# Kernel optimization log

Measured on AMD Instinct MI355X. Metric: run time of the kernel, lower is better.

## Reference

```python
import jax, jax.numpy as jnp
import numpy as np

CURVE = 1.0
TAU = 0.5
N_NODES = 32768
N_EDGES = 65536
IN_CH = 64
OUT_CH = 64
N_HEADS = 8
N_RF = 128
EPS = 1e-7


def _make_projection_matrix(m, d, seed=0):
    # FAVOR+ projection: stacked rows of transposed QR blocks, row-rescaled by chi norms.
    rng = np.random.RandomState(seed)
    blocks = []
    nb_full = m // d
    for _ in range(nb_full):
        q, _ = np.linalg.qr(rng.randn(d, d))
        blocks.append(q.T)
    rem = m - nb_full * d
    if rem > 0:
        q, _ = np.linalg.qr(rng.randn(d, d))
        blocks.append(q.T[:rem])
    final = np.vstack(blocks)  # [m, d]
    mult = np.linalg.norm(rng.randn(m, d), axis=1)
    return (mult[:, None] * final).astype(np.float32)


def _expmap0(u, c):
    # Hyperboloid exp map at origin; time slot of u is ignored.
    sqrtK = 1.0 / jnp.sqrt(c)
    x = u[..., 1:]
    xn = jnp.maximum(jnp.linalg.norm(x, axis=-1, keepdims=True), EPS)
    theta = xn / sqrtK
    return jnp.concatenate([sqrtK * jnp.cosh(theta), sqrtK * jnp.sinh(theta) * x / xn], axis=-1)


def _proj(x, c):
    # Re-project onto hyperboloid: x0 = sqrt(1/c + ||x_space||^2)
    K = 1.0 / c
    y = x[..., 1:]
    t = jnp.sqrt(K + jnp.sum(y * y, axis=-1, keepdims=True))
    return jnp.concatenate([t, y], axis=-1)


def _logmap0(x, c):
    # Hyperboloid log map at origin; output tangent has zero time component.
    sqrtK = 1.0 / jnp.sqrt(c)
    y = x[..., 1:]
    yn = jnp.maximum(jnp.linalg.norm(y, axis=-1, keepdims=True), EPS)
    t = jnp.maximum(x[..., 0:1] / sqrtK, 1.0 + EPS)
    res = sqrtK * jnp.arccosh(t) * y / yn
    return jnp.concatenate([jnp.zeros_like(res[..., :1]), res], axis=-1)


def _softmax_kernel(data, P, tau, c):
    # Performer-style exp kernel with hyperbolic (time-coordinate) prefactor.
    dt = data[..., 0:1]
    ds = data[..., 1:]
    m = 1.0 / jnp.sqrt(jnp.asarray(P.shape[0], jnp.float32))
    wx = jnp.exp(jnp.einsum('bnhd,dm->bnhm', ds, P) / jnp.sqrt(tau))
    front = jnp.exp((c / tau - dt * dt / tau) / 2.0) * m  # [b,n,h,1]
    return wx * front


def setup_inputs() -> dict:
    key = jax.random.key(0)
    k1, k2, k3, k4 = jax.random.split(key, 4)
    std = (2.0 / (IN_CH + OUT_CH)) ** 0.5
    z = 0.01 * jax.random.normal(k1, (1, N_NODES, IN_CH), jnp.float32)
    Wq = std * jax.random.normal(k2, (N_HEADS, OUT_CH, IN_CH), jnp.float32)
    Wk = std * jax.random.normal(k3, (N_HEADS, OUT_CH, IN_CH), jnp.float32)
    Wv = std * jax.random.normal(k4, (N_HEADS, OUT_CH, IN_CH), jnp.float32)
    edge_index = jax.random.randint(jax.random.fold_in(key, 7), (2, N_EDGES), 0, N_NODES, jnp.int32)
    proj_mat = jnp.asarray(_make_projection_matrix(IN_CH - 1, N_RF))  # [63, 128]
    return {"z": z, "Wq": Wq, "Wk": Wk, "Wv": Wv, "proj_mat": proj_mat, "edge_index": edge_index}


def reference(z, Wq, Wk, Wv, proj_mat, edge_index):
    c = jnp.float32(CURVE)
    tau = jnp.float32(TAU)
    zs = z[0]  # [N, C] (B == 1, squeeze)
    zh = _proj(_expmap0(zs, c), c)  # lift features to hyperboloid
    u = _logmap0(zh, c)             # [N, C], tangent at origin

    def hyplin(W):  # HypLinear (no bias): proj(expmap0(logmap0(x) @ W^T)) for all heads
        mu = jnp.einsum('nc,hoc->hno', u, W)  # [H, N, D]
        return _proj(_expmap0(mu, c), c)

    q, k, v = hyplin(Wq), hyplin(Wk), hyplin(Wv)  # [H, N, D]
    H, N, D = q.shape
    # mirrors torch stacked.reshape(-1, N, H, D) (row-major relabeling)
    query = q.reshape(1, N, H, D)
    key_ = k.reshape(1, N, H, D)
    value = v.reshape(1, N, H, D)

    qp = _softmax_kernel(query, proj_mat, tau, c).transpose(2, 0, 1, 3)  # [H,1,N,M]
    kp = _softmax_kernel(key_, proj_mat, tau, c).transpose(2, 0, 1, 3)   # [H,1,N,M]
    vv = value.transpose(2, 0, 1, 3)                                      # [H,1,N,D]

    last = jnp.einsum('hbnm,hbnd->hbmd', kp, vv)   # [H,1,M,D] kv summary
    zo = jnp.einsum('hbnm,hbmd->hbnd', qp, last)   # [H,1,N,D]
    mnorm = -zo[..., 0:1] ** 2 + jnp.sum(zo[..., 1:] ** 2, axis=-1, keepdims=True)
    zo = zo / (jnp.sqrt(c) * jnp.sqrt(jnp.abs(mnorm)))  # renormalize onto hyperboloid

    start, end = edge_index[0], edge_index[1]
    ea = jnp.einsum('hbem,hbem->hbe', qp[:, :, end, :], kp[:, :, start, :])
    A_weight = ea.transpose(1, 2, 0)  # [1, E, H]

    # hyper_agg: Euclidean head-mean followed by Minkowski renormalization
    t = jnp.mean(zo[:, 0], axis=0)  # [N, D]
    xn = -t[..., 0:1] ** 2 + jnp.sum(t[..., 1:] ** 2, axis=-1, keepdims=True)
    z_next = t / (jnp.sqrt(c) * jnp.sqrt(jnp.abs(xn)))
    link_loss = jnp.mean(A_weight)
    return z_next, link_loss
```

## Files before the change

kernel.cpp:

```cpp
#include <hip/hip_runtime.h>

#define DEV __device__ __forceinline__

#define NNODES 32768
#define NEDGES 65536
#define NROWS  262144
#define EPSF   1e-7f
#define SQRT2F 1.4142135623730951f
#define LOG2E  1.4426950408889634f
#define LOG2SQRT63 2.9886399611087573f

#define OFF_WFRAG 0u
#define OFF_LASTB 0u
#define OFF_PFRAG 196608u
#define OFF_EA    212992u
#define OFF_U     409600u
#define OFF_PART  42352640u
#define OFF_PHIQ  75907072u
#define OFF_PHIK  143015936u

typedef short s8v __attribute__((ext_vector_type(8)));
typedef float f4v __attribute__((ext_vector_type(4)));
typedef float f2v __attribute__((ext_vector_type(2)));

DEV unsigned short f2bf(float f) {
  unsigned u = __float_as_uint(f);
  return (unsigned short)((u + 0x7fffu + ((u >> 16) & 1u)) >> 16);
}
DEV float bf2f(unsigned short h) { return __uint_as_float(((unsigned)h) << 16); }
DEV unsigned pack2(float lo, float hi) {
  return __builtin_amdgcn_perm(__float_as_uint(hi) + 0x8000u, __float_as_uint(lo) + 0x8000u, 0x07060302u);
}
DEV float frcp(float x) { return __builtin_amdgcn_rcpf(x); }
DEV float fsqrt(float x) { return __builtin_amdgcn_sqrtf(x); }
DEV float fexp2(float x) { return __builtin_amdgcn_exp2f(x); }

__global__ __launch_bounds__(256) void k01_prep(const float* __restrict__ z, unsigned short* __restrict__ ubf,
                                                const float* __restrict__ Wq, const float* __restrict__ Wk,
                                                const float* __restrict__ Wv, const float* __restrict__ P,
                                                unsigned short* __restrict__ Wfrag, unsigned short* __restrict__ Pfrag,
                                                float* __restrict__ ea) {
  int i = blockIdx.x * 256 + threadIdx.x;
  float4 v = *(const float4*)(z + (size_t)i * 4);
  if ((i & 15) == 0) v.x = 0.f;
  uint2 pk;
  pk.x = pack2(v.x, v.y);
  pk.y = pack2(v.z, v.w);
  *(uint2*)(ubf + (size_t)i * 4) = pk;

  if (blockIdx.x < 96) {
    if (i == 0) ea[0] = 0.f;
    int stride = 96 * 256;
    for (int t = i; t < 98304; t += stride) {
      int j = t & 7, lane = (t >> 3) & 63, nt = (t >> 9) & 3, ks = (t >> 11) & 1, h = (t >> 12) & 7, sm = t >> 15;
      int k = ks * 32 + (lane >> 4) * 8 + j;
      int n = nt * 16 + (lane & 15);
      const float* W = (sm == 0) ? Wq : ((sm == 1) ? Wk : Wv);
      Wfrag[t] = f2bf(W[(h * 64 + n) * 64 + k]);
    }
    for (int t = i; t < 8192; t += stride) {
      int j = t & 7, lane = (t >> 3) & 63, ks = (t >> 9) & 1, mt = (t >> 10) & 7;
      int k = ks * 32 + (lane >> 4) * 8 + j;
      int r = lane & 15;
      int m = ((mt >> 2) << 6) + ((r >> 2) << 4) + ((mt & 3) << 2) + (r & 3);
      Pfrag[t] = (k == 0) ? (unsigned short)0 : f2bf(P[(k - 1) * 128 + m] * (SQRT2F * LOG2E));
    }
  }
}

__global__ __launch_bounds__(256, 4) void k2_mfma(const unsigned short* __restrict__ ubf,
                                                  const unsigned short* __restrict__ Wfrag,
                                                  const unsigned short* __restrict__ Pfrag,
                                                  unsigned char* __restrict__ phiq, unsigned char* __restrict__ phik,
                                                  unsigned short* __restrict__ part) {
  __shared__ short lds_raw[13312];
  short* sbuf = lds_raw;
  float* sfront = (float*)(lds_raw + 9216);
  unsigned char* kbufT8 = (unsigned char*)lds_raw;
  unsigned char* vbufT8 = (unsigned char*)lds_raw + 9216;

  int w = threadIdx.x >> 6, lane = threadIdx.x & 63;
  int q = lane >> 4, l = lane & 15;
  int b = blockIdx.x;
  int h = b >> 8, t = b & 255;
  int n0 = t * 128 + w * 32;

  s8v afr[2][2];
#pragma unroll
  for (int mt = 0; mt < 2; ++mt)
#pragma unroll
    for (int ks = 0; ks < 2; ++ks)
      afr[mt][ks] = *(const s8v*)(ubf + (size_t)(n0 + mt * 16 + l) * 64 + ks * 32 + q * 8);

  const s8v* Wf = (const s8v*)Wfrag;
  const s8v* Pf = (const s8v*)Pfrag;
  unsigned vk[2][4];
  unsigned keepA[8], keepB[8];

#pragma unroll
  for (int sm = 0; sm < 3; ++sm) {
    f4v acc[2][4];
#pragma unroll
    for (int mt = 0; mt < 2; ++mt)
#pragma unroll
      for (int nt = 0; nt < 4; ++nt) acc[mt][nt] = (f4v)(0.f);
#pragma unroll
    for (int ks = 0; ks < 2; ++ks)
#pragma unroll
      for (int nt = 0; nt < 4; ++nt) {
        s8v bf = Wf[(((sm * 8 + h) * 2 + ks) * 4 + nt) * 64 + lane];
#pragma unroll
        for (int mt = 0; mt < 2; ++mt)
          acc[mt][nt] = __builtin_amdgcn_mfma_f32_16x16x32_bf16(afr[mt][ks], bf, acc[mt][nt], 0, 0, 0);
      }
#pragma unroll
    for (int mt = 0; mt < 2; ++mt) {
      float rs[4];
#pragma unroll
      for (int reg = 0; reg < 4; ++reg) {
        float v0 = (l == 0) ? 0.f : acc[mt][0][reg];
        rs[reg] = v0 * v0 + acc[mt][1][reg] * acc[mt][1][reg] + acc[mt][2][reg] * acc[mt][2][reg] +
                  acc[mt][3][reg] * acc[mt][3][reg];
      }
#pragma unroll
      for (int reg = 0; reg < 4; ++reg) {
#pragma unroll
        for (int off = 1; off < 16; off <<= 1) rs[reg] += __shfl_xor(rs[reg], off, 64);
      }
      float vreg[4][4];
#pragma unroll
      for (int reg = 0; reg < 4; ++reg) {
        float x = fmaxf(fsqrt(rs[reg]), EPSF);
        float e = fexp2(x * LOG2E);
        float sh = 0.5f * (e - frcp(e));
        float ratio = sh * frcp(x);
        float sh2 = sh * sh;
        int row = mt * 16 + q * 4 + reg;
        if (sm == 2) {
          float tt2 = fsqrt(1.f + sh2);
#pragma unroll
          for (int nt = 0; nt < 4; ++nt) {
            float val = acc[mt][nt][reg] * ratio;
            if (l == 0 && nt == 0) val = tt2;
            vreg[nt][reg] = val;
          }
        } else {
          float lf = -sh2 * LOG2E - LOG2SQRT63;
          if (l == 0) sfront[w * 32 + row] = lf;
#pragma unroll
          for (int nt = 0; nt < 4; ++nt) {
            float val = acc[mt][nt][reg] * ratio;
            if (l == 0 && nt == 0) val = 0.f;
            sbuf[w * 2304 + row * 72 + ((nt * 16 + l) ^ ((q >> 1) << 4))] =
                (short)(__float_as_uint(val) >> 16);
          }
        }
      }
      if (sm == 2) {
#pragma unroll
        for (int nt = 0; nt < 4; ++nt) {
          unsigned pv = __builtin_amdgcn_cvt_pk_fp8_f32(vreg[nt][0], vreg[nt][1], 0, 0);
          vk[mt][nt] = __builtin_amdgcn_cvt_pk_fp8_f32(vreg[nt][2], vreg[nt][3], pv, 1);
        }
      }
    }

    if (sm < 2) {
      int fr = (l >> 3) & 1;
      s8v bsf[2][2];
#pragma unroll
      for (int nt = 0; nt < 2; ++nt)
#pragma unroll
        for (int ks = 0; ks < 2; ++ks)
          bsf[nt][ks] = *(const s8v*)&sbuf[w * 2304 + (nt * 16 + l) * 72 + ((ks * 32 + q * 8) ^ (fr << 4))];
      float lf0 = sfront[w * 32 + l];
      float lf1 = sfront[w * 32 + 16 + l];
      unsigned char* dst = sm ? phik : phiq;
      unsigned g0a[4], g0b[4], g1a[4], g1b[4];
#pragma unroll
      for (int mt = 0; mt < 8; ++mt) {
        f4v a0 = (f4v)(0.f), a1 = (f4v)(0.f);
#pragma unroll
        for (int ks = 0; ks < 2; ++ks) {
          s8v ap = Pf[(mt * 2 + ks) * 64 + lane];
          a0 = __builtin_amdgcn_mfma_f32_16x16x32_bf16(ap, bsf[0][ks], a0, 0, 0, 0);
          a1 = __builtin_amdgcn_mfma_f32_16x16x32_bf16(ap, bsf[1][ks], a1, 0, 0, 0);
        }
        float v00 = fexp2(a0[0] + lf0), v01 = fexp2(a0[1] + lf0), v02 = fexp2(a0[2] + lf0), v03 = fexp2(a0[3] + lf0);
        float v10 = fexp2(a1[0] + lf1), v11 = fexp2(a1[1] + lf1), v12 = fexp2(a1[2] + lf1), v13 = fexp2(a1[3] + lf1);
        unsigned p0 = __builtin_amdgcn_cvt_pk_fp8_f32(v00, v01, 0, 0);
        p0 = __builtin_amdgcn_cvt_pk_fp8_f32(v02, v03, p0, 1);
        unsigned p1 = __builtin_amdgcn_cvt_pk_fp8_f32(v10, v11, 0, 0);
        p1 = __builtin_amdgcn_cvt_pk_fp8_f32(v12, v13, p1, 1);
        if (mt < 4) { g0a[mt] = p0; g1a[mt] = p1; }
        else        { g0b[mt - 4] = p0; g1b[mt - 4] = p1; }
        if (sm == 1) { keepA[mt] = p0; keepB[mt] = p1; }
      }
      size_t b0 = (size_t)(n0 + l) * 1024 + (size_t)(h * 128 + q * 16);
      *(uint4*)(dst + b0)              = make_uint4(g0a[0], g0a[1], g0a[2], g0a[3]);
      *(uint4*)(dst + b0 + 64)         = make_uint4(g0b[0], g0b[1], g0b[2], g0b[3]);
      *(uint4*)(dst + b0 + 16384)      = make_uint4(g1a[0], g1a[1], g1a[2], g1a[3]);
      *(uint4*)(dst + b0 + 16384 + 64) = make_uint4(g1b[0], g1b[1], g1b[2], g1b[3]);
    }
  }

  f4v facc[2][4];
#pragma unroll
  for (int mtl = 0; mtl < 2; ++mtl)
#pragma unroll
    for (int nt = 0; nt < 4; ++nt) facc[mtl][nt] = (f4v)(0.f);

#pragma unroll
  for (int hf = 0; hf < 2; ++hf) {
    __syncthreads();
    if ((w >> 1) == hf) {
      int nd0 = (w & 1) * 32 + l, nd1 = nd0 + 16;
      int c0 = nd0 ^ (q << 4), c1 = nd1 ^ (q << 4);
#pragma unroll
      for (int mt = 0; mt < 8; ++mt) {
        int M0 = ((mt >> 2) << 6) + (q << 4) + ((mt & 3) << 2);
        unsigned a = keepA[mt], bq = keepB[mt];
#pragma unroll
        for (int r = 0; r < 4; ++r) {
          kbufT8[(M0 + r) * 72 + c0] = (unsigned char)(a >> (8 * r));
          kbufT8[(M0 + r) * 72 + c1] = (unsigned char)(bq >> (8 * r));
        }
      }
#pragma unroll
      for (int mt = 0; mt < 2; ++mt)
#pragma unroll
        for (int nt = 0; nt < 4; ++nt)
          *(unsigned*)&vbufT8[(nt * 16 + l) * 72 + (w & 1) * 32 + mt * 16 + q * 4] = vk[mt][nt];
    }
    __syncthreads();
#pragma unroll
    for (int kc = 0; kc < 2; ++kc) {
      long bv[4];
#pragma unroll
      for (int nt = 0; nt < 4; ++nt)
        bv[nt] = *(const long*)&vbufT8[(nt * 16 + l) * 72 + kc * 32 + q * 8];
      long av[2];
#pragma unroll
      for (int mtl = 0; mtl < 2; ++mtl) {
        int row = (2 * w + mtl) * 16 + l;
        int cb = (kc * 32 + q * 8) ^ (((2 * w + mtl) & 3) << 4);
        av[mtl] = *(const long*)&kbufT8[row * 72 + cb];
      }
#pragma unroll
      for (int mtl = 0; mtl < 2; ++mtl)
#pragma unroll
        for (int nt = 0; nt < 4; ++nt)
          facc[mtl][nt] = __builtin_amdgcn_mfma_f32_16x16x32_fp8_fp8(av[mtl], bv[nt], facc[mtl][nt], 0, 0, 0);
    }
  }

#pragma unroll
  for (int mtl = 0; mtl < 2; ++mtl)
#pragma unroll
    for (int nt = 0; nt < 4; ++nt) {
      uint2 pk;
      pk.x = pack2(facc[mtl][nt][0], facc[mtl][nt][1]);
      pk.y = pack2(facc[mtl][nt][2], facc[mtl][nt][3]);
      int d = nt * 16 + l;
      int m = (2 * w + mtl) * 16 + q * 4;
      *(uint2*)(part + ((size_t)((t * 8 + h) * 64 + d)) * 128 + m) = pk;
    }
}

__global__ __launch_bounds__(256) void k35(const unsigned* __restrict__ part32, unsigned char* __restrict__ lastB,
                                           const unsigned char* __restrict__ phiq,
                                           const unsigned char* __restrict__ phik,
                                           const int* __restrict__ ei, float* __restrict__ ea) {
  int b = blockIdx.x;
  if (b < 128) {
    int t2 = b * 256 + threadIdx.x;
    float s0 = 0.f, s1 = 0.f;
#pragma unroll 16
    for (int c = 0; c < 256; ++c) {
      unsigned v = part32[((size_t)c << 12) + t2];
      s0 += __uint_as_float(v << 16);
      s1 += __uint_as_float(v & 0xffff0000u);
    }
    int m = (t2 & 63) * 2, d = (t2 >> 6) & 63, h = t2 >> 12;
    int ks = m >> 5, j = m & 7, qq = (m >> 3) & 3;
    int lane = qq * 16 + (d & 15), nt = d >> 4;
    unsigned r = __builtin_amdgcn_cvt_pk_bf8_f32(s0, s1, 0, 0);
    *(unsigned short*)(lastB + ((((h * 4 + ks) * 4 + nt) * 64 + lane) << 3) + j) = (unsigned short)r;
    return;
  }
  __shared__ float part[4];
  int lane = threadIdx.x & 63, w = threadIdx.x >> 6;
  int wid = (b - 128) * 4 + w;
  float acc0 = 0.f, acc1 = 0.f;
#pragma unroll
  for (int i = 0; i < 8; i += 2) {
    int e0 = wid * 8 + i, e1 = e0 + 1;
    int s0 = ei[e0], d0 = ei[NEDGES + e0];
    int s1 = ei[e1], d1 = ei[NEDGES + e1];
    uint4 qa = *(const uint4*)(phiq + (size_t)d0 * 1024 + lane * 16);
    uint4 ka = *(const uint4*)(phik + (size_t)s0 * 1024 + lane * 16);
    uint4 qb = *(const uint4*)(phiq + (size_t)d1 * 1024 + lane * 16);
    uint4 kb = *(const uint4*)(phik + (size_t)s1 * 1024 + lane * 16);
    unsigned qs[8] = {qa.x, qa.y, qa.z, qa.w, qb.x, qb.y, qb.z, qb.w};
    unsigned ks[8] = {ka.x, ka.y, ka.z, ka.w, kb.x, kb.y, kb.z, kb.w};
#pragma unroll
    for (int p = 0; p < 8; ++p) {
      f2v q0 = __builtin_amdgcn_cvt_pk_f32_fp8(qs[p], 0);
      f2v q1 = __builtin_amdgcn_cvt_pk_f32_fp8(qs[p], 1);
      f2v k0 = __builtin_amdgcn_cvt_pk_f32_fp8(ks[p], 0);
      f2v k1 = __builtin_amdgcn_cvt_pk_f32_fp8(ks[p], 1);
      float t0 = fmaf(q0.x, k0.x, q0.y * k0.y);
      float t1 = fmaf(q1.x, k1.x, q1.y * k1.y);
      if (p < 4) acc0 += t0 + t1; else acc1 += t0 + t1;
    }
  }
  float acc = acc0 + acc1;
#pragma unroll
  for (int o = 1; o < 64; o <<= 1) acc += __shfl_xor(acc, o, 64);
  if (lane == 0) part[w] = acc;
  __syncthreads();
  if (threadIdx.x == 0) atomicAdd(ea, part[0] + part[1] + part[2] + part[3]);
}

__global__ __launch_bounds__(512) void k4_mfma(const unsigned char* __restrict__ phiq,
                                               const unsigned char* __restrict__ lastB,
                                               const float* __restrict__ ea, float* __restrict__ out) {
  __shared__ unsigned zbufT[8][64][18];
  int w = threadIdx.x >> 6, lane = threadIdx.x & 63;
  int q = lane >> 4, l = lane & 15;
  int n0 = blockIdx.x * 32;

  const long* Bf = (const long*)lastB;
  long bf[4][4];
#pragma unroll
  for (int ks = 0; ks < 4; ++ks)
#pragma unroll
    for (int nt = 0; nt < 4; ++nt) bf[ks][nt] = Bf[((w * 4 + ks) * 4 + nt) * 64 + lane];

  long af[2][4];
#pragma unroll
  for (int mt = 0; mt < 2; ++mt)
#pragma unroll
    for (int ks = 0; ks < 4; ++ks)
      af[mt][ks] = *(const long*)(phiq + (size_t)(8 * (n0 + mt * 16 + l) + w) * 128 + ks * 32 + q * 8);

  f4v acc[2][4];
#pragma unroll
  for (int mt = 0; mt < 2; ++mt)
#pragma unroll
    for (int nt = 0; nt < 4; ++nt) acc[mt][nt] = (f4v)(0.f);
#pragma unroll
  for (int ks = 0; ks < 4; ++ks)
#pragma unroll
    for (int nt = 0; nt < 4; ++nt)
#pragma unroll
      for (int mt = 0; mt < 2; ++mt)
        acc[mt][nt] = __builtin_amdgcn_mfma_f32_16x16x32_fp8_bf8(af[mt][ks], bf[ks][nt], acc[mt][nt], 0, 0, 0);

#pragma unroll
  for (int mt = 0; mt < 2; ++mt) {
    float rs[4];
#pragma unroll
    for (int reg = 0; reg < 4; ++reg) {
      float v0 = acc[mt][0][reg];
      float s0 = (l == 0) ? -v0 * v0 : v0 * v0;
      rs[reg] = s0 + acc[mt][1][reg] * acc[mt][1][reg] + acc[mt][2][reg] * acc[mt][2][reg] +
                acc[mt][3][reg] * acc[mt][3][reg];
    }
#pragma unroll
    for (int reg = 0; reg < 4; ++reg) {
#pragma unroll
      for (int off = 1; off < 16; off <<= 1) rs[reg] += __shfl_xor(rs[reg], off, 64);
    }
    float inv[4];
#pragma unroll
    for (int reg = 0; reg < 4; ++reg) inv[reg] = frcp(fsqrt(fabsf(rs[reg])));
#pragma unroll
    for (int nt = 0; nt < 4; ++nt) {
      uint2 pk;
      pk.x = pack2(acc[mt][nt][0] * inv[0], acc[mt][nt][1] * inv[1]);
      pk.y = pack2(acc[mt][nt][2] * inv[2], acc[mt][nt][3] * inv[3]);
      *(uint2*)&zbufT[w][nt * 16 + l][mt * 8 + q * 2] = pk;
    }
  }
  __syncthreads();

  int tid = threadIdx.x;
  int i = tid >> 4, dg = tid & 15;
  int i2 = i >> 1, sel = i & 1;
  float s[4] = {0.f, 0.f, 0.f, 0.f};
#pragma unroll
  for (int w2 = 0; w2 < 8; ++w2) {
#pragma unroll
    for (int j = 0; j < 4; ++j) {
      unsigned u = zbufT[w2][dg * 4 + j][i2];
      s[j] += bf2f((unsigned short)(sel ? (u >> 16) : (u & 0xffffu)));
    }
  }
  float m2 = 0.f;
#pragma unroll
  for (int j = 0; j < 4; ++j) {
    s[j] *= 0.125f;
    m2 += ((dg == 0 && j == 0) ? -s[j] * s[j] : s[j] * s[j]);
  }
#pragma unroll
  for (int off = 1; off < 16; off <<= 1) m2 += __shfl_xor(m2, off, 64);
  float inv = frcp(fsqrt(fabsf(m2)));
  float4 o = make_float4(s[0] * inv, s[1] * inv, s[2] * inv, s[3] * inv);
  *(float4*)(out + (size_t)(n0 + i) * 64 + dg * 4) = o;
  if (blockIdx.x == 0 && tid == 0) out[(size_t)NNODES * 64] = ea[0] * (1.0f / 524288.0f);
}

extern "C" void kernel_launch(void* const* d_in, const int* in_sizes, int n_in,
                              void* d_out, int out_size, void* d_ws, size_t ws_size,
                              hipStream_t stream) {
  const float* z  = (const float*)d_in[0];
  const float* Wq = (const float*)d_in[1];
  const float* Wk = (const float*)d_in[2];
  const float* Wv = (const float*)d_in[3];
  const float* P  = (const float*)d_in[4];
  const int* ei   = (const int*)d_in[5];
  char* ws = (char*)d_ws;
  unsigned short* Wfrag = (unsigned short*)(ws + OFF_WFRAG);
  unsigned char*  lastB = (unsigned char*)(ws + OFF_LASTB);
  unsigned short* Pfrag = (unsigned short*)(ws + OFF_PFRAG);
  float*          ea    = (float*)(ws + OFF_EA);
  unsigned short* ubf   = (unsigned short*)(ws + OFF_U);
  unsigned short* part  = (unsigned short*)(ws + OFF_PART);
  unsigned char*  phiq  = (unsigned char*)(ws + OFF_PHIQ);
  unsigned char*  phik  = (unsigned char*)(ws + OFF_PHIK);

  k01_prep<<<2048, 256, 0, stream>>>(z, ubf, Wq, Wk, Wv, P, Wfrag, Pfrag, ea);
  k2_mfma<<<2048, 256, 0, stream>>>(ubf, Wfrag, Pfrag, phiq, phik, part);
  k35<<<128 + 2048, 256, 0, stream>>>((const unsigned*)part, lastB, phiq, phik, ei, ea);
  k4_mfma<<<NNODES / 32, 512, 0, stream>>>(phiq, lastB, ea, (float*)d_out);
}
```

Before: 177.4 us.

## Store per-tile KV partial sums as bf8 and shrink LDS for higher occupancy

The per-tile K^T V partial sums written by k2 are now packed to bf8 instead of bf16, halving that intermediate buffer, and the k35 reduction reads four bf8 values per word, so it launches half as many reduction blocks. The k2 LDS array is cut down and launch bounds raised from 4 to 8 blocks per CU to allow more occupancy. The cost is extra quantization error in 256 partial sums summed into the kv summary, and the smaller LDS array may be inconsistent with kbufT8/vbufT8 regions that previously extended beyond it.

```diff
diff --git a/kernel.cpp b/kernel.cpp
--- a/kernel.cpp
+++ b/kernel.cpp
@@ -68,12 +68,12 @@
   }
 }
 
-__global__ __launch_bounds__(256, 4) void k2_mfma(const unsigned short* __restrict__ ubf,
+__global__ __launch_bounds__(256, 8) void k2_mfma(const unsigned short* __restrict__ ubf,
                                                   const unsigned short* __restrict__ Wfrag,
                                                   const unsigned short* __restrict__ Pfrag,
                                                   unsigned char* __restrict__ phiq, unsigned char* __restrict__ phik,
-                                                  unsigned short* __restrict__ part) {
-  __shared__ short lds_raw[13312];
+                                                  unsigned char* __restrict__ part8) {
+  __shared__ short lds_raw[9472];
   short* sbuf = lds_raw;
   float* sfront = (float*)(lds_raw + 9216);
   unsigned char* kbufT8 = (unsigned char*)lds_raw;
@@ -258,12 +258,11 @@
   for (int mtl = 0; mtl < 2; ++mtl)
 #pragma unroll
     for (int nt = 0; nt < 4; ++nt) {
-      uint2 pk;
-      pk.x = pack2(facc[mtl][nt][0], facc[mtl][nt][1]);
-      pk.y = pack2(facc[mtl][nt][2], facc[mtl][nt][3]);
+      unsigned pk8 = __builtin_amdgcn_cvt_pk_bf8_f32(facc[mtl][nt][0], facc[mtl][nt][1], 0, 0);
+      pk8 = __builtin_amdgcn_cvt_pk_bf8_f32(facc[mtl][nt][2], facc[mtl][nt][3], pk8, 1);
       int d = nt * 16 + l;
       int m = (2 * w + mtl) * 16 + q * 4;
-      *(uint2*)(part + ((size_t)((t * 8 + h) * 64 + d)) * 128 + m) = pk;
+      *(unsigned*)(part8 + ((size_t)((t * 8 + h) * 64 + d)) * 128 + m) = pk8;
     }
 }
 
@@ -272,25 +271,28 @@
                                            const unsigned char* __restrict__ phik,
                                            const int* __restrict__ ei, float* __restrict__ ea) {
   int b = blockIdx.x;
-  if (b < 128) {
+  if (b < 64) {
     int t2 = b * 256 + threadIdx.x;
-    float s0 = 0.f, s1 = 0.f;
-#pragma unroll 16
+    float s0 = 0.f, s1 = 0.f, s2 = 0.f, s3 = 0.f;
+#pragma unroll 8
     for (int c = 0; c < 256; ++c) {
-      unsigned v = part32[((size_t)c << 12) + t2];
-      s0 += __uint_as_float(v << 16);
-      s1 += __uint_as_float(v & 0xffff0000u);
-    }
-    int m = (t2 & 63) * 2, d = (t2 >> 6) & 63, h = t2 >> 12;
-    int ks = m >> 5, j = m & 7, qq = (m >> 3) & 3;
+      unsigned v = part32[(c << 14) + t2];
+      f2v lo = __builtin_amdgcn_cvt_pk_f32_bf8(v, 0);
+      f2v hi = __builtin_amdgcn_cvt_pk_f32_bf8(v, 1);
+      s0 += lo.x; s1 += lo.y; s2 += hi.x; s3 += hi.y;
+    }
+    int mq = t2 & 31, d = (t2 >> 5) & 63, h = t2 >> 11;
+    int m0 = mq * 4;
+    int ks = m0 >> 5, j0 = m0 & 7, qq = (m0 >> 3) & 3;
     int lane = qq * 16 + (d & 15), nt = d >> 4;
     unsigned r = __builtin_amdgcn_cvt_pk_bf8_f32(s0, s1, 0, 0);
-    *(unsigned short*)(lastB + ((((h * 4 + ks) * 4 + nt) * 64 + lane) << 3) + j) = (unsigned short)r;
+    r = __builtin_amdgcn_cvt_pk_bf8_f32(s2, s3, r, 1);
+    *(unsigned*)(lastB + ((((h * 4 + ks) * 4 + nt) * 64 + lane) << 3) + j0) = r;
     return;
   }
   __shared__ float part[4];
   int lane = threadIdx.x & 63, w = threadIdx.x >> 6;
-  int wid = (b - 128) * 4 + w;
+  int wid = (b - 64) * 4 + w;
   float acc0 = 0.f, acc1 = 0.f;
 #pragma unroll
   for (int i = 0; i < 8; i += 2) {
@@ -426,12 +428,12 @@
   unsigned short* Pfrag = (unsigned short*)(ws + OFF_PFRAG);
   float*          ea    = (float*)(ws + OFF_EA);
   unsigned short* ubf   = (unsigned short*)(ws + OFF_U);
-  unsigned short* part  = (unsigned short*)(ws + OFF_PART);
+  unsigned char*  part8 = (unsigned char*)(ws + OFF_PART);
   unsigned char*  phiq  = (unsigned char*)(ws + OFF_PHIQ);
   unsigned char*  phik  = (unsigned char*)(ws + OFF_PHIK);
 
   k01_prep<<<2048, 256, 0, stream>>>(z, ubf, Wq, Wk, Wv, P, Wfrag, Pfrag, ea);
-  k2_mfma<<<2048, 256, 0, stream>>>(ubf, Wfrag, Pfrag, phiq, phik, part);
-  k35<<<128 + 2048, 256, 0, stream>>>((const unsigned*)part, lastB, phiq, phik, ei, ea);
+  k2_mfma<<<2048, 256, 0, stream>>>(ubf, Wfrag, Pfrag, phiq, phik, part8);
+  k35<<<64 + 2048, 256, 0, stream>>>((const unsigned*)part8, lastB, phiq, phik, ei, ea);
   k4_mfma<<<NNODES / 32, 512, 0, stream>>>(phiq, lastB, ea, (float*)d_out);
 }
```

Measured after the change: 254.8 us. +43.7%, slower.
